# Kernel tuning notes

Measured on AMD Instinct MI355X. Metric: run time of the kernel, lower is better.

The kernel has to match this reference:

```python
import jax, jax.numpy as jnp
import numpy as np

B, N, C = 4, 4096, 512
H = 8          # num_heads
M = 64         # num_landmarks
HD = C // H    # head_dim = 64
N_ITER = 6     # Newton-Schulz iterations (Nystromformer default)


def iterative_inv(mat):
    # mat: [B, H, M, M]; Nystromformer pseudo-inverse via Newton-Schulz.
    I = jnp.eye(mat.shape[-1], dtype=mat.dtype)
    K = mat
    # global-max initialization (original Nystromformer 'original' init)
    V = K.swapaxes(-1, -2) / (jnp.max(jnp.sum(K, axis=-2)) * jnp.max(jnp.sum(K, axis=-1)))
    for _ in range(N_ITER):
        KV = jnp.matmul(K, V)
        V = 0.25 * jnp.matmul(V, 13.0 * I - jnp.matmul(KV, 15.0 * I - jnp.matmul(KV, 7.0 * I - KV)))
    return V


def setup_inputs() -> dict:
    key = jax.random.key(0)
    k1, k2, k3, k4 = jax.random.split(key, 4)
    s = C ** -0.5
    return {
        "x": jax.random.normal(k1, (B, N, C), dtype=jnp.float32),
        "qkv_w": jax.random.normal(k2, (3 * C, C), dtype=jnp.float32) * s,
        "proj_w": jax.random.normal(k3, (C, C), dtype=jnp.float32) * s,
        "proj_b": jax.random.normal(k4, (C,), dtype=jnp.float32) * 0.01,
        "epoch": 1,
    }


def reference(x, qkv_w, proj_w, proj_b, epoch):
    b, n, c = x.shape
    hd = c // H
    qkv = (x @ qkv_w.T).reshape(b, n, 3, H, hd).transpose(2, 0, 3, 1, 4)  # [3,B,H,N,hd]
    Q, K, V = qkv[0], qkv[1], qkv[2]
    scale = 1.0 / np.sqrt(np.sqrt(hd)).astype(np.float32)
    Q = Q * scale
    K = K * scale
    # landmark pooling: mean over segments of length N // M
    Ql = Q.reshape(b, H, M, n // M, hd).mean(axis=-2)  # [B,H,M,hd]
    Kl = K.reshape(b, H, M, n // M, hd).mean(axis=-2)
    kernel_1 = jax.nn.softmax(jnp.einsum('bhnd,bhmd->bhnm', Q, Kl), axis=-1)   # [B,H,N,M]
    kernel_2 = jax.nn.softmax(jnp.einsum('bhmd,bhld->bhml', Ql, Kl), axis=-1)  # [B,H,M,M]
    kernel_3 = jax.nn.softmax(jnp.einsum('bhmd,bhnd->bhmn', Ql, K), axis=-1)   # [B,H,M,N]
    X = jnp.matmul(jnp.matmul(kernel_1, iterative_inv(kernel_2)), jnp.matmul(kernel_3, V))
    X = X.transpose(0, 2, 1, 3).reshape(b, n, c)
    return X @ proj_w.T + proj_b
```

## Files before the change

kernel.cpp:

```cpp
#include <hip/hip_runtime.h>
#include <hip/hip_bf16.h>
#include <stdint.h>

#define QSZe 8388608ull

typedef __attribute__((ext_vector_type(8))) short bf16x8;
typedef __attribute__((ext_vector_type(4))) float f32x4;
typedef const __attribute__((address_space(1))) unsigned int* gas1_t;
typedef __attribute__((address_space(3))) unsigned int* las3_t;

__device__ __forceinline__ float bf2f(unsigned short u) {
  return __uint_as_float(((unsigned int)u) << 16);
}
__device__ __forceinline__ unsigned short f2bf(float f) {
  unsigned int u = __float_as_uint(f);
  unsigned int r = (u + 0x7FFFu + ((u >> 16) & 1u)) >> 16;
  return (unsigned short)r;
}
__device__ __forceinline__ void gload_lds16(const void* g, void* l) {
  __builtin_amdgcn_global_load_lds((gas1_t)g, (las3_t)l, 16, 0, 0);
}

__global__ void detect_dtype(const unsigned short* __restrict__ raw,
                             unsigned int* __restrict__ flag) {
  int t = threadIdx.x;
  int big = 0;
  for (int i = t; i < 256; i += 64) {
    int e = (raw[i] >> 7) & 0xFF;
    if (e >= 0x8F) big = 1;
  }
  unsigned long long b = __ballot(big);
  if (t == 0) flag[0] = (b != 0ull) ? 1u : 0u;
}

__global__ __launch_bounds__(256) void convert_bf16(
    const void* __restrict__ raw, unsigned short* __restrict__ canon, int n,
    const unsigned int* __restrict__ flag) {
  int i8 = (blockIdx.x * 256 + threadIdx.x) * 8;
  if (i8 >= n) return;
  if (flag[0]) {
    const float* f = (const float*)raw;
    float4 a = *(const float4*)(f + i8);
    float4 b = *(const float4*)(f + i8 + 4);
    unsigned short o[8] = {f2bf(a.x), f2bf(a.y), f2bf(a.z), f2bf(a.w),
                           f2bf(b.x), f2bf(b.y), f2bf(b.z), f2bf(b.w)};
    *(uint4*)(canon + i8) = *(const uint4*)o;
  } else {
    *(uint4*)(canon + i8) = *(const uint4*)((const unsigned short*)raw + i8);
  }
}

__global__ __launch_bounds__(256) void convert_f32(
    const void* __restrict__ raw, float* __restrict__ canon, int n,
    const unsigned int* __restrict__ flag) {
  int i = blockIdx.x * 256 + threadIdx.x;
  if (i >= n) return;
  canon[i] = flag[0] ? ((const float*)raw)[i]
                     : bf2f(((const unsigned short*)raw)[i]);
}

__device__ __forceinline__ void mmB(const unsigned short* A_R,
                                    const unsigned short* B_T,
                                    unsigned short* out_R,
                                    unsigned short* out_T, int wave, int lane,
                                    float s, float dg, float a7,
                                    const unsigned short* Aelt) {
  const int fr = lane & 15, fq = lane >> 4;
  bf16x8 af0 = *(const bf16x8*)&A_R[(wave * 16 + fr) * 64 + fq * 8];
  bf16x8 af1 = *(const bf16x8*)&A_R[(wave * 16 + fr) * 64 + 32 + fq * 8];
  f32x4 acc[4] = {};
#pragma unroll
  for (int j = 0; j < 4; j++) {
    bf16x8 b0 = *(const bf16x8*)&B_T[(j * 16 + fr) * 64 + fq * 8];
    bf16x8 b1 = *(const bf16x8*)&B_T[(j * 16 + fr) * 64 + 32 + fq * 8];
    acc[j] = __builtin_amdgcn_mfma_f32_16x16x32_bf16(af0, b0, acc[j], 0, 0, 0);
    acc[j] = __builtin_amdgcn_mfma_f32_16x16x32_bf16(af1, b1, acc[j], 0, 0, 0);
  }
  float ael[4][4];
  if (Aelt) {
#pragma unroll
    for (int j = 0; j < 4; j++)
#pragma unroll
      for (int r = 0; r < 4; r++)
        ael[j][r] = bf2f(Aelt[(wave * 16 + fq * 4 + r) * 64 + j * 16 + fr]);
  }
  __syncthreads();
#pragma unroll
  for (int j = 0; j < 4; j++) {
    int col = j * 16 + fr;
    unsigned short pack[4];
#pragma unroll
    for (int r = 0; r < 4; r++) {
      int row = wave * 16 + fq * 4 + r;
      float v = s * acc[j][r] + ((row == col) ? dg : 0.0f);
      if (Aelt) v += a7 * ael[j][r];
      unsigned short bv = f2bf(v);
      if (out_R) out_R[row * 64 + col] = bv;
      pack[r] = bv;
    }
    if (out_T)
      *(uint2*)&out_T[col * 64 + wave * 16 + fq * 4] = *(const uint2*)pack;
  }
}

__global__ __launch_bounds__(256) void qkv_gemm_mfma(
    const unsigned short* __restrict__ x, const unsigned short* __restrict__ w,
    unsigned short* __restrict__ qkv) {
  __shared__ __align__(16) unsigned short At[128 * 64];
  __shared__ __align__(16) unsigned short Bt[128 * 64];
  const int t = threadIdx.x;
  const int lane = t & 63, wave = t >> 6;
  const int wr = wave >> 1, wc = wave & 1;
  const int i0 = blockIdx.y * 128, j0 = blockIdx.x * 128;
  const int srow = lane >> 3;
  const int skc = (lane & 7) * 8;
  const int fr = lane & 15, fq = lane >> 4;
  f32x4 acc[4][4] = {};

  for (int k0 = 0; k0 < 512; k0 += 64) {
#pragma unroll
    for (int s = 0; s < 4; s++) {
      int inst = wave * 4 + s;
      int row = inst * 8 + srow;
      gload_lds16(x + (size_t)(i0 + row) * 512 + k0 + skc, &At[inst * 512]);
      gload_lds16(w + (size_t)(j0 + row) * 512 + k0 + skc, &Bt[inst * 512]);
    }
    __syncthreads();
#pragma unroll
    for (int kk = 0; kk < 64; kk += 32) {
      bf16x8 af[4], bg[4];
#pragma unroll
      for (int i = 0; i < 4; i++)
        af[i] = *(const bf16x8*)&At[(wr * 64 + i * 16 + fr) * 64 + kk + fq * 8];
#pragma unroll
      for (int j = 0; j < 4; j++)
        bg[j] = *(const bf16x8*)&Bt[(wc * 64 + j * 16 + fr) * 64 + kk + fq * 8];
#pragma unroll
      for (int i = 0; i < 4; i++)
#pragma unroll
        for (int j = 0; j < 4; j++)
          acc[i][j] = __builtin_amdgcn_mfma_f32_16x16x32_bf16(
              af[i], bg[j], acc[i][j], 0, 0, 0);
    }
    __syncthreads();
  }
#pragma unroll
  for (int j = 0; j < 4; j++) {
    int col = j0 + wc * 64 + j * 16 + fr;
    int which = col >> 9;
    int h = (col >> 6) & 7;
    int d = col & 63;
    float scale = (which < 2) ? 0.3535533905932738f : 1.0f;
#pragma unroll
    for (int i = 0; i < 4; i++) {
      int rbase = i0 + wr * 64 + i * 16 + fq * 4;
#pragma unroll
      for (int r = 0; r < 4; r++) {
        int row = rbase + r;
        int b_ = row >> 12, n = row & 4095;
        qkv[(size_t)which * QSZe + ((size_t)(b_ * 8 + h) * 4096 + n) * 64 + d] =
            f2bf(acc[i][j][r] * scale);
      }
    }
  }
}

__global__ __launch_bounds__(256) void pool_kernel(
    const unsigned short* __restrict__ qkv, float* __restrict__ Ql,
    float* __restrict__ Kl, unsigned short* __restrict__ Klb,
    unsigned short* __restrict__ Qlb) {
  int idx = blockIdx.x * 256 + threadIdx.x;
  int d = idx & 63;
  int m = (idx >> 6) & 63;
  int bh = idx >> 12;
  const unsigned short* qb =
      qkv + (size_t)bh * 262144 + (size_t)m * 4096 + d;
  const unsigned short* kb = qb + QSZe;
  float sq = 0.f, sk = 0.f;
#pragma unroll 8
  for (int tok = 0; tok < 64; tok++) {
    sq += bf2f(qb[tok * 64]);
    sk += bf2f(kb[tok * 64]);
  }
  float qv = sq * (1.0f / 64.0f);
  float kv = sk * (1.0f / 64.0f);
  Ql[idx] = qv;
  Kl[idx] = kv;
  Klb[idx] = f2bf(kv);
  Qlb[idx] = f2bf(qv);
}

__global__ __launch_bounds__(256) void k2_kernel(
    const float* __restrict__ Ql, const float* __restrict__ Kl,
    float* __restrict__ k2, unsigned int* __restrict__ gstat) {
  __shared__ float KlT[64 * 64];
  __shared__ float Ps[64][65];
  int t = threadIdx.x;
  int lane = t & 63, wv = t >> 6;
  int bh = blockIdx.x;
#pragma unroll
  for (int i = 0; i < 16; i++) {
    int idx = i * 256 + t;
    KlT[(idx & 63) * 64 + (idx >> 6)] = Kl[bh * 4096 + idx];
  }
  __syncthreads();
  for (int r = wv * 16; r < wv * 16 + 16; r++) {
    float qv = Ql[(bh * 64 + r) * 64 + lane];
    float acc = 0.f;
#pragma unroll
    for (int k = 0; k < 64; k++) acc += __shfl(qv, k, 64) * KlT[k * 64 + lane];
    float mx = acc;
#pragma unroll
    for (int o = 32; o > 0; o >>= 1) mx = fmaxf(mx, __shfl_xor(mx, o, 64));
    float e = __expf(acc - mx);
    float s = e;
#pragma unroll
    for (int o = 32; o > 0; o >>= 1) s += __shfl_xor(s, o, 64);
    float p = e / s;
    k2[(bh * 64 + r) * 64 + lane] = p;
    Ps[r][lane] = p;
  }
  __syncthreads();
  float val = 0.f;
  if (t < 64) {
    for (int r = 0; r < 64; r++) val += Ps[r][t];
  } else if (t < 128) {
    int r = t - 64;
    for (int c = 0; c < 64; c++) val += Ps[r][c];
  }
  float mv = val;
#pragma unroll
  for (int o = 32; o > 0; o >>= 1) mv = fmaxf(mv, __shfl_xor(mv, o, 64));
  if (t == 0) atomicMax(gstat + 0, __float_as_uint(mv));
  if (t == 64) atomicMax(gstat + 1, __float_as_uint(mv));
}

__global__ __launch_bounds__(256) void k3_mfma(
    const unsigned short* __restrict__ Qlb,
    const unsigned short* __restrict__ qkv, float* __restrict__ Wp,
    float* __restrict__ sp) {
  __shared__ __align__(16) unsigned short Et[64 * 136];
  __shared__ __align__(16) unsigned short Vt[64 * 136];
  __shared__ float scol_l[4][64];
  const int t = threadIdx.x;
  const int lane = t & 63, wave = t >> 6;
  const int fr = lane & 15, fq = lane >> 4;
  const int slab = blockIdx.x, bh = blockIdx.y;
  const int n_base = slab * 512;
  const unsigned short* Kb = qkv + QSZe + (size_t)bh * 262144;
  const unsigned short* Vb = qkv + 2 * QSZe + (size_t)bh * 262144;
  const unsigned short* Qlp = Qlb + bh * 4096;

  bf16x8 qb[2][4];
#pragma unroll
  for (int h = 0; h < 2; h++)
#pragma unroll
    for (int j = 0; j < 4; j++)
      qb[h][j] = *(const bf16x8*)(Qlp + (j * 16 + fr) * 64 + h * 32 + fq * 8);

  f32x4 accW[4] = {};
  float scol[4] = {0.f, 0.f, 0.f, 0.f};

  for (int sc = 0; sc < 4; sc++) {
    const int n0 = n_base + sc * 128;
    {
      int n = t & 127, dg = t >> 7;
#pragma unroll
      for (int i = 0; i < 4; i++) {
        int d0 = (dg + 2 * i) * 8;
        uint4 v = *(const uint4*)(Vb + (size_t)(n0 + n) * 64 + d0);
        const unsigned short* s = (const unsigned short*)&v;
#pragma unroll
        for (int u = 0; u < 8; u++) Vt[(d0 + u) * 136 + n] = s[u];
      }
    }
    f32x4 acc[2][4] = {};
#pragma unroll
    for (int i = 0; i < 2; i++) {
      const unsigned short* Kr =
          Kb + (size_t)(n0 + wave * 32 + i * 16 + fr) * 64;
      bf16x8 a0 = *(const bf16x8*)(Kr + fq * 8);
      bf16x8 a1 = *(const bf16x8*)(Kr + 32 + fq * 8);
#pragma unroll
      for (int j = 0; j < 4; j++) {
        acc[i][j] =
            __builtin_amdgcn_mfma_f32_16x16x32_bf16(a0, qb[0][j], acc[i][j],
                                                    0, 0, 0);
        acc[i][j] =
            __builtin_amdgcn_mfma_f32_16x16x32_bf16(a1, qb[1][j], acc[i][j],
                                                    0, 0, 0);
      }
    }
#pragma unroll
    for (int i = 0; i < 2; i++)
#pragma unroll
      for (int j = 0; j < 4; j++) {
        unsigned short pack[4];
        float s4 = 0.f;
#pragma unroll
        for (int r = 0; r < 4; r++) {
          float e = __expf(acc[i][j][r]);
          s4 += e;
          pack[r] = f2bf(e);
        }
        scol[j] += s4;
        *(uint2*)&Et[(j * 16 + fr) * 136 + wave * 32 + i * 16 + fq * 4] =
            *(const uint2*)pack;
      }
    __syncthreads();
#pragma unroll
    for (int kk = 0; kk < 128; kk += 32) {
      bf16x8 ap = *(const bf16x8*)&Et[(wave * 16 + fr) * 136 + kk + fq * 8];
#pragma unroll
      for (int j = 0; j < 4; j++) {
        bf16x8 bv = *(const bf16x8*)&Vt[(j * 16 + fr) * 136 + kk + fq * 8];
        accW[j] =
            __builtin_amdgcn_mfma_f32_16x16x32_bf16(ap, bv, accW[j], 0, 0, 0);
      }
    }
    __syncthreads();
  }
#pragma unroll
  for (int j = 0; j < 4; j++) {
    float s = scol[j];
    s += __shfl_xor(s, 16, 64);
    s += __shfl_xor(s, 32, 64);
    if (fq == 0) scol_l[wave][j * 16 + fr] = s;
  }
  __syncthreads();
  if (t < 64)
    sp[(bh * 8 + slab) * 64 + t] =
        scol_l[0][t] + scol_l[1][t] + scol_l[2][t] + scol_l[3][t];
  float* wpo = Wp + ((size_t)bh * 8 + slab) * 4096;
#pragma unroll
  for (int j = 0; j < 4; j++)
#pragma unroll
    for (int r = 0; r < 4; r++)
      wpo[(wave * 16 + fq * 4 + r) * 64 + j * 16 + fr] = accW[j][r];
}

__global__ __launch_bounds__(256) void k3_reduce(
    const float* __restrict__ Wp, const float* __restrict__ sp,
    float* __restrict__ W) {
  int idx = blockIdx.x * 256 + threadIdx.x;
  int m = (idx >> 6) & 63, bh = idx >> 12;
  float w = 0.f, s = 0.f;
#pragma unroll
  for (int c = 0; c < 8; c++) {
    w += Wp[((size_t)bh * 8 + c) * 4096 + (idx & 4095)];
    s += sp[(bh * 8 + c) * 64 + m];
  }
  W[idx] = w / s;
}

__global__ __launch_bounds__(256) void ns_kernel(
    const float* __restrict__ k2g, const unsigned int* __restrict__ gstat,
    const float* __restrict__ Wg, unsigned short* __restrict__ Ztb) {
  __shared__ __align__(16) unsigned short L[8 * 4096];
  unsigned short* K2R = L;
  unsigned short* VR = L + 4096;
  unsigned short* VT = L + 2 * 4096;
  unsigned short* AR = L + 3 * 4096;
  unsigned short* AT = L + 4 * 4096;
  unsigned short* T2T = L + 5 * 4096;
  unsigned short* T3T = L + 6 * 4096;
  unsigned short* WT = L + 7 * 4096;
  const int t = threadIdx.x, bh = blockIdx.x;
  const int lane = t & 63, wave = t >> 6;
  const float scale =
      1.0f / (__uint_as_float(gstat[0]) * __uint_as_float(gstat[1]));
  const float* k2p = k2g + bh * 4096;
  const float* wp = Wg + bh * 4096;
#pragma unroll
  for (int i = 0; i < 16; i++) {
    int idx = i * 256 + t;
    int r = idx >> 6, c = idx & 63;
    float kv = k2p[idx];
    K2R[idx] = f2bf(kv);
    VT[idx] = f2bf(kv * scale);
    VR[idx] = f2bf(k2p[c * 64 + r] * scale);
    WT[idx] = f2bf(wp[c * 64 + r]);
  }
  __syncthreads();
  for (int it = 0; it < 6; it++) {
    mmB(K2R, VT, AR, AT, wave, lane, 1.0f, 0.0f, 0.0f, nullptr);
    __syncthreads();
    mmB(AR, AT, nullptr, T2T, wave, lane, 1.0f, 15.0f, -7.0f, AR);
    __syncthreads();
    mmB(AR, T2T, nullptr, T3T, wave, lane, -1.0f, 13.0f, 0.0f, nullptr);
    __syncthreads();
    mmB(VR, T3T, VR, VT, wave, lane, 0.25f, 0.0f, 0.0f, nullptr);
    __syncthreads();
  }
  {
    const int fr = lane & 15, fq = lane >> 4;
    bf16x8 af0 = *(const bf16x8*)&WT[(wave * 16 + fr) * 64 + fq * 8];
    bf16x8 af1 = *(const bf16x8*)&WT[(wave * 16 + fr) * 64 + 32 + fq * 8];
    f32x4 acc[4] = {};
#pragma unroll
    for (int j = 0; j < 4; j++) {
      bf16x8 b0 = *(const bf16x8*)&VR[(j * 16 + fr) * 64 + fq * 8];
      bf16x8 b1 = *(const bf16x8*)&VR[(j * 16 + fr) * 64 + 32 + fq * 8];
      acc[j] =
          __builtin_amdgcn_mfma_f32_16x16x32_bf16(af0, b0, acc[j], 0, 0, 0);
      acc[j] =
          __builtin_amdgcn_mfma_f32_16x16x32_bf16(af1, b1, acc[j], 0, 0, 0);
    }
#pragma unroll
    for (int j = 0; j < 4; j++) {
      int m = j * 16 + fr;
#pragma unroll
      for (int r = 0; r < 4; r++) {
        int d = wave * 16 + fq * 4 + r;
        Ztb[bh * 4096 + d * 64 + m] = f2bf(acc[j][r]);
      }
    }
  }
}

__global__ __launch_bounds__(256) void k1x_mfma(
    const unsigned short* __restrict__ qkv,
    const unsigned short* __restrict__ Klb,
    const unsigned short* __restrict__ Ztb, unsigned short* __restrict__ X) {
  __shared__ __align__(16) unsigned short Qt[128 * 64];
  __shared__ __align__(16) unsigned short Ps[128 * 72];
  const int t = threadIdx.x;
  const int lane = t & 63, wave = t >> 6;
  const int fr = lane & 15, fq = lane >> 4;
  const int bh = blockIdx.x;
  const int n0 = blockIdx.y * 128;
  const unsigned short* Qb = qkv + (size_t)bh * 262144 + (size_t)n0 * 64;
  const unsigned short* Klp = Klb + bh * 4096;
  const unsigned short* Ztp = Ztb + bh * 4096;

  {
    const int srow = lane >> 3, skc = (lane & 7) * 8;
#pragma unroll
    for (int s = 0; s < 4; s++) {
      int inst = wave * 4 + s;
      gload_lds16(Qb + (size_t)(inst * 8 + srow) * 64 + skc, &Qt[inst * 512]);
    }
  }
  __syncthreads();

  f32x4 acc[2][4] = {};
#pragma unroll
  for (int kk = 0; kk < 64; kk += 32) {
    bf16x8 af[2], bg[4];
#pragma unroll
    for (int i = 0; i < 2; i++)
      af[i] =
          *(const bf16x8*)&Qt[(wave * 32 + i * 16 + fr) * 64 + kk + fq * 8];
#pragma unroll
    for (int j = 0; j < 4; j++)
      bg[j] = *(const bf16x8*)(Klp + (j * 16 + fr) * 64 + kk + fq * 8);
#pragma unroll
    for (int i = 0; i < 2; i++)
#pragma unroll
      for (int j = 0; j < 4; j++)
        acc[i][j] = __builtin_amdgcn_mfma_f32_16x16x32_bf16(af[i], bg[j],
                                                            acc[i][j], 0, 0, 0);
  }

#pragma unroll
  for (int i = 0; i < 2; i++) {
    float sr[4] = {0.f, 0.f, 0.f, 0.f};
#pragma unroll
    for (int j = 0; j < 4; j++)
#pragma unroll
      for (int r = 0; r < 4; r++) {
        float e = __expf(acc[i][j][r]);
        acc[i][j][r] = e;
        sr[r] += e;
      }
#pragma unroll
    for (int mask = 1; mask < 16; mask <<= 1)
#pragma unroll
      for (int r = 0; r < 4; r++) sr[r] += __shfl_xor(sr[r], mask, 64);
    float is[4];
#pragma unroll
    for (int r = 0; r < 4; r++) is[r] = 1.0f / sr[r];
#pragma unroll
    for (int j = 0; j < 4; j++)
#pragma unroll
      for (int r = 0; r < 4; r++)
        Ps[(wave * 32 + i * 16 + fq * 4 + r) * 72 + j * 16 + fr] =
            f2bf(acc[i][j][r] * is[r]);
  }
  __syncthreads();

  f32x4 ax[2][4] = {};
#pragma unroll
  for (int kk = 0; kk < 64; kk += 32) {
    bf16x8 ap[2], bz[4];
#pragma unroll
    for (int i = 0; i < 2; i++)
      ap[i] =
          *(const bf16x8*)&Ps[(wave * 32 + i * 16 + fr) * 72 + kk + fq * 8];
#pragma unroll
    for (int j = 0; j < 4; j++)
      bz[j] = *(const bf16x8*)(Ztp + (j * 16 + fr) * 64 + kk + fq * 8);
#pragma unroll
    for (int i = 0; i < 2; i++)
#pragma unroll
      for (int j = 0; j < 4; j++)
        ax[i][j] = __builtin_amdgcn_mfma_f32_16x16x32_bf16(ap[i], bz[j],
                                                           ax[i][j], 0, 0, 0);
  }

  const int b_ = bh >> 3, h = bh & 7;
#pragma unroll
  for (int i = 0; i < 2; i++) {
#pragma unroll
    for (int j = 0; j < 4; j++) {
      int c = h * 64 + j * 16 + fr;
#pragma unroll
      for (int r = 0; r < 4; r++) {
        int n = n0 + wave * 32 + i * 16 + fq * 4 + r;
        X[((size_t)(b_ * 4096 + n)) * 512 + c] = f2bf(ax[i][j][r]);
      }
    }
  }
}

__global__ __launch_bounds__(256) void proj_gemm_mfma(
    const unsigned short* __restrict__ X, const unsigned short* __restrict__ w,
    const float* __restrict__ bias, float* __restrict__ out) {
  __shared__ __align__(16) unsigned short At[128 * 64];
  __shared__ __align__(16) unsigned short Bt[128 * 64];
  const int t = threadIdx.x;
  const int lane = t & 63, wave = t >> 6;
  const int wr = wave >> 1, wc = wave & 1;
  const int i0 = blockIdx.y * 128, j0 = blockIdx.x * 128;
  const int srow = lane >> 3;
  const int skc = (lane & 7) * 8;
  const int fr = lane & 15, fq = lane >> 4;
  f32x4 acc[4][4] = {};

  for (int k0 = 0; k0 < 512; k0 += 64) {
#pragma unroll
    for (int s = 0; s < 4; s++) {
      int inst = wave * 4 + s;
      int row = inst * 8 + srow;
      gload_lds16(X + (size_t)(i0 + row) * 512 + k0 + skc, &At[inst * 512]);
      gload_lds16(w + (size_t)(j0 + row) * 512 + k0 + skc, &Bt[inst * 512]);
    }
    __syncthreads();
#pragma unroll
    for (int kk = 0; kk < 64; kk += 32) {
      bf16x8 af[4], bg[4];
#pragma unroll
      for (int i = 0; i < 4; i++)
        af[i] = *(const bf16x8*)&At[(wr * 64 + i * 16 + fr) * 64 + kk + fq * 8];
#pragma unroll
      for (int j = 0; j < 4; j++)
        bg[j] = *(const bf16x8*)&Bt[(wc * 64 + j * 16 + fr) * 64 + kk + fq * 8];
#pragma unroll
      for (int i = 0; i < 4; i++)
#pragma unroll
        for (int j = 0; j < 4; j++)
          acc[i][j] = __builtin_amdgcn_mfma_f32_16x16x32_bf16(
              af[i], bg[j], acc[i][j], 0, 0, 0);
    }
    __syncthreads();
  }
#pragma unroll
  for (int j = 0; j < 4; j++) {
    int col = j0 + wc * 64 + j * 16 + fr;
    float bia = bias[col];
#pragma unroll
    for (int i = 0; i < 4; i++) {
      int rbase = i0 + wr * 64 + i * 16 + fq * 4;
#pragma unroll
      for (int r = 0; r < 4; r++) {
        out[(size_t)(rbase + r) * 512 + col] = acc[i][j][r] + bia;
      }
    }
  }
}

extern "C" void kernel_launch(void* const* d_in, const int* in_sizes, int n_in,
                              void* d_out, int out_size, void* d_ws,
                              size_t ws_size, hipStream_t stream) {
  (void)in_sizes; (void)n_in; (void)out_size; (void)ws_size;

  char* w8 = (char*)d_ws;
  unsigned short* cx  = (unsigned short*)(w8 + 0);
  unsigned short* cwq = (unsigned short*)(w8 + 16777216);
  unsigned short* cwp = (unsigned short*)(w8 + 18350080);
  float*          cbf = (float*)(w8 + 18874368);
  unsigned short* qkv = (unsigned short*)(w8 + 18876416);
  unsigned short* X   = (unsigned short*)(w8 + 69208064);
  float* Ql = (float*)(w8 + 85985280);
  float* Kl = (float*)(w8 + 86509568);
  float* k2 = (float*)(w8 + 87033856);
  float* W  = (float*)(w8 + 87558144);
  unsigned short* Ztb = (unsigned short*)(w8 + 88082432);
  unsigned int* gstat = (unsigned int*)(w8 + 88606720);
  float* Wp = (float*)(w8 + 88608768);
  float* sp = (float*)(w8 + 92803072);
  unsigned short* Klb = (unsigned short*)(w8 + 92868608);
  unsigned short* Qlb = (unsigned short*)(w8 + 93130752);

  hipMemsetAsync(gstat, 0, 16, stream);
  detect_dtype<<<1, 64, 0, stream>>>((const unsigned short*)d_in[0],
                                     gstat + 2);
  convert_bf16<<<4096, 256, 0, stream>>>(d_in[0], cx, 8388608, gstat + 2);
  convert_bf16<<<384, 256, 0, stream>>>(d_in[1], cwq, 786432, gstat + 2);
  convert_bf16<<<128, 256, 0, stream>>>(d_in[2], cwp, 262144, gstat + 2);
  convert_f32<<<2, 256, 0, stream>>>(d_in[3], cbf, 512, gstat + 2);

  qkv_gemm_mfma<<<dim3(12, 128), 256, 0, stream>>>(cx, cwq, qkv);
  pool_kernel<<<512, 256, 0, stream>>>(qkv, Ql, Kl, Klb, Qlb);
  k2_kernel<<<32, 256, 0, stream>>>(Ql, Kl, k2, gstat);
  k3_mfma<<<dim3(8, 32), 256, 0, stream>>>(Qlb, qkv, Wp, sp);
  k3_reduce<<<512, 256, 0, stream>>>(Wp, sp, W);
  ns_kernel<<<32, 256, 0, stream>>>(k2, gstat, W, Ztb);
  k1x_mfma<<<dim3(32, 32), 256, 0, stream>>>(qkv, Klb, Ztb, X);
  proj_gemm_mfma<<<dim3(4, 128), 256, 0, stream>>>(X, cwp, cbf,
                                                   (float*)d_out);
}
```

Baseline: 255.3 us.

## Fuse landmark pooling into QKV GEMM epilogue and merge conversion/reduce kernels

The QKV GEMM is transposed so each wave's accumulator tile covers a whole 64-token segment of one head. The epilogue can then compute the landmark means by a cross-lane shuffle reduction and write Ql/Kl directly, which removes the separate pool kernel's re-read of Q and K. The epilogue also writes qkv as packed 4-element stores along the head dimension. In addition, the three bf16 conversions become one kernel, bias conversion moves into the dtype-detect kernel, and the k3_reduce kernel is folded into the ns_kernel prologue, cutting launches and an intermediate buffer. The risk is extra shuffle and register work in the GEMM epilogue, plus the ns_kernel prologue now doing eight strided global reads per element.

```diff
diff --git a/kernel.cpp b/kernel.cpp
--- a/kernel.cpp
+++ b/kernel.cpp
@@ -21,42 +21,57 @@
   __builtin_amdgcn_global_load_lds((gas1_t)g, (las3_t)l, 16, 0, 0);
 }
 
-__global__ void detect_dtype(const unsigned short* __restrict__ raw,
-                             unsigned int* __restrict__ flag) {
+__global__ void detect_bias(const unsigned short* __restrict__ raw_x,
+                            const void* __restrict__ raw_b,
+                            float* __restrict__ cbf,
+                            unsigned int* __restrict__ flag) {
+  __shared__ unsigned int fl;
   int t = threadIdx.x;
-  int big = 0;
-  for (int i = t; i < 256; i += 64) {
-    int e = (raw[i] >> 7) & 0xFF;
-    if (e >= 0x8F) big = 1;
-  }
-  unsigned long long b = __ballot(big);
-  if (t == 0) flag[0] = (b != 0ull) ? 1u : 0u;
-}
-
-__global__ __launch_bounds__(256) void convert_bf16(
-    const void* __restrict__ raw, unsigned short* __restrict__ canon, int n,
+  if (t < 64) {
+    int big = 0;
+    for (int i = t; i < 256; i += 64) {
+      int e = (raw_x[i] >> 7) & 0xFF;
+      if (e >= 0x8F) big = 1;
+    }
+    unsigned long long b = __ballot(big);
+    if (t == 0) {
+      fl = (b != 0ull) ? 1u : 0u;
+      flag[0] = fl;
+    }
+  }
+  __syncthreads();
+  unsigned int f = fl;
+  for (int i = t; i < 512; i += 256)
+    cbf[i] = f ? ((const float*)raw_b)[i]
+               : bf2f(((const unsigned short*)raw_b)[i]);
+}
+
+__global__ __launch_bounds__(256) void conv_all(
+    const void* __restrict__ rx, const void* __restrict__ rwq,
+    const void* __restrict__ rwp, unsigned short* __restrict__ cx,
+    unsigned short* __restrict__ cwq, unsigned short* __restrict__ cwp,
     const unsigned int* __restrict__ flag) {
-  int i8 = (blockIdx.x * 256 + threadIdx.x) * 8;
-  if (i8 >= n) return;
+  int gid = blockIdx.x * 256 + threadIdx.x;
+  const void* src;
+  unsigned short* dst;
+  int i8;
+  if (gid < 1048576) {
+    src = rx; dst = cx; i8 = gid * 8;
+  } else if (gid < 1146880) {
+    src = rwq; dst = cwq; i8 = (gid - 1048576) * 8;
+  } else {
+    src = rwp; dst = cwp; i8 = (gid - 1146880) * 8;
+  }
   if (flag[0]) {
-    const float* f = (const float*)raw;
+    const float* f = (const float*)src;
     float4 a = *(const float4*)(f + i8);
     float4 b = *(const float4*)(f + i8 + 4);
     unsigned short o[8] = {f2bf(a.x), f2bf(a.y), f2bf(a.z), f2bf(a.w),
                            f2bf(b.x), f2bf(b.y), f2bf(b.z), f2bf(b.w)};
-    *(uint4*)(canon + i8) = *(const uint4*)o;
+    *(uint4*)(dst + i8) = *(const uint4*)o;
   } else {
-    *(uint4*)(canon + i8) = *(const uint4*)((const unsigned short*)raw + i8);
-  }
-}
-
-__global__ __launch_bounds__(256) void convert_f32(
-    const void* __restrict__ raw, float* __restrict__ canon, int n,
-    const unsigned int* __restrict__ flag) {
-  int i = blockIdx.x * 256 + threadIdx.x;
-  if (i >= n) return;
-  canon[i] = flag[0] ? ((const float*)raw)[i]
-                     : bf2f(((const unsigned short*)raw)[i]);
+    *(uint4*)(dst + i8) = *(const uint4*)((const unsigned short*)src + i8);
+  }
 }
 
 __device__ __forceinline__ void mmB(const unsigned short* A_R,
@@ -104,16 +119,17 @@
 }
 
 __global__ __launch_bounds__(256) void qkv_gemm_mfma(
-    const unsigned short* __restrict__ x, const unsigned short* __restrict__ w,
-    unsigned short* __restrict__ qkv) {
+    const unsigned short* __restrict__ w, const unsigned short* __restrict__ x,
+    unsigned short* __restrict__ qkv, float* __restrict__ Ql,
+    float* __restrict__ Kl, unsigned short* __restrict__ Qlb,
+    unsigned short* __restrict__ Klb) {
   __shared__ __align__(16) unsigned short At[128 * 64];
   __shared__ __align__(16) unsigned short Bt[128 * 64];
   const int t = threadIdx.x;
   const int lane = t & 63, wave = t >> 6;
-  const int wr = wave >> 1, wc = wave & 1;
-  const int i0 = blockIdx.y * 128, j0 = blockIdx.x * 128;
-  const int srow = lane >> 3;
-  const int skc = (lane & 7) * 8;
+  const int wf = wave >> 1, wt = wave & 1;
+  const int f0 = blockIdx.x * 128, n0g = blockIdx.y * 128;
+  const int srow = lane >> 3, skc = (lane & 7) * 8;
   const int fr = lane & 15, fq = lane >> 4;
   f32x4 acc[4][4] = {};
 
@@ -122,72 +138,76 @@
     for (int s = 0; s < 4; s++) {
       int inst = wave * 4 + s;
       int row = inst * 8 + srow;
-      gload_lds16(x + (size_t)(i0 + row) * 512 + k0 + skc, &At[inst * 512]);
-      gload_lds16(w + (size_t)(j0 + row) * 512 + k0 + skc, &Bt[inst * 512]);
+      gload_lds16(w + (size_t)(f0 + row) * 512 + k0 + skc, &At[inst * 512]);
+      gload_lds16(x + (size_t)(n0g + row) * 512 + k0 + skc, &Bt[inst * 512]);
     }
     __syncthreads();
 #pragma unroll
     for (int kk = 0; kk < 64; kk += 32) {
-      bf16x8 af[4], bg[4];
+      bf16x8 af[4], bxf[4];
 #pragma unroll
       for (int i = 0; i < 4; i++)
-        af[i] = *(const bf16x8*)&At[(wr * 64 + i * 16 + fr) * 64 + kk + fq * 8];
+        af[i] = *(const bf16x8*)&At[(wf * 64 + i * 16 + fr) * 64 + kk + fq * 8];
 #pragma unroll
       for (int j = 0; j < 4; j++)
-        bg[j] = *(const bf16x8*)&Bt[(wc * 64 + j * 16 + fr) * 64 + kk + fq * 8];
+        bxf[j] =
+            *(const bf16x8*)&Bt[(wt * 64 + j * 16 + fr) * 64 + kk + fq * 8];
 #pragma unroll
       for (int i = 0; i < 4; i++)
 #pragma unroll
         for (int j = 0; j < 4; j++)
           acc[i][j] = __builtin_amdgcn_mfma_f32_16x16x32_bf16(
-              af[i], bg[j], acc[i][j], 0, 0, 0);
-    }
-    __syncthreads();
-  }
-#pragma unroll
-  for (int j = 0; j < 4; j++) {
-    int col = j0 + wc * 64 + j * 16 + fr;
-    int which = col >> 9;
-    int h = (col >> 6) & 7;
-    int d = col & 63;
-    float scale = (which < 2) ? 0.3535533905932738f : 1.0f;
+              af[i], bxf[j], acc[i][j], 0, 0, 0);
+    }
+    __syncthreads();
+  }
+  const int fbase = f0 + wf * 64;
+  const int which = fbase >> 9;
+  const int h = (fbase >> 6) & 7;
+  const float scale = (which < 2) ? 0.3535533905932738f : 1.0f;
+  const int b_ = n0g >> 12;
+  const int bh = b_ * 8 + h;
+  const int m_loc = ((n0g + wt * 64) & 4095) >> 6;
+#pragma unroll
+  for (int i = 0; i < 4; i++) {
+    int d0 = i * 16 + fq * 4;
+#pragma unroll
+    for (int j = 0; j < 4; j++) {
+      int nn = (n0g + wt * 64 + j * 16 + fr) & 4095;
+      unsigned short pack[4];
+#pragma unroll
+      for (int r = 0; r < 4; r++) pack[r] = f2bf(acc[i][j][r] * scale);
+      *(uint2*)&qkv[(size_t)which * QSZe + ((size_t)bh * 4096 + nn) * 64 +
+                    d0] = *(const uint2*)pack;
+    }
+  }
+  if (which < 2) {
+    const float ps = scale * (1.0f / 64.0f);
 #pragma unroll
     for (int i = 0; i < 4; i++) {
-      int rbase = i0 + wr * 64 + i * 16 + fq * 4;
-#pragma unroll
-      for (int r = 0; r < 4; r++) {
-        int row = rbase + r;
-        int b_ = row >> 12, n = row & 4095;
-        qkv[(size_t)which * QSZe + ((size_t)(b_ * 8 + h) * 4096 + n) * 64 + d] =
-            f2bf(acc[i][j][r] * scale);
-      }
-    }
-  }
-}
-
-__global__ __launch_bounds__(256) void pool_kernel(
-    const unsigned short* __restrict__ qkv, float* __restrict__ Ql,
-    float* __restrict__ Kl, unsigned short* __restrict__ Klb,
-    unsigned short* __restrict__ Qlb) {
-  int idx = blockIdx.x * 256 + threadIdx.x;
-  int d = idx & 63;
-  int m = (idx >> 6) & 63;
-  int bh = idx >> 12;
-  const unsigned short* qb =
-      qkv + (size_t)bh * 262144 + (size_t)m * 4096 + d;
-  const unsigned short* kb = qb + QSZe;
-  float sq = 0.f, sk = 0.f;
-#pragma unroll 8
-  for (int tok = 0; tok < 64; tok++) {
-    sq += bf2f(qb[tok * 64]);
-    sk += bf2f(kb[tok * 64]);
-  }
-  float qv = sq * (1.0f / 64.0f);
-  float kv = sk * (1.0f / 64.0f);
-  Ql[idx] = qv;
-  Kl[idx] = kv;
-  Klb[idx] = f2bf(kv);
-  Qlb[idx] = f2bf(qv);
+      float sm[4];
+#pragma unroll
+      for (int r = 0; r < 4; r++)
+        sm[r] = acc[i][0][r] + acc[i][1][r] + acc[i][2][r] + acc[i][3][r];
+#pragma unroll
+      for (int mask = 1; mask < 16; mask <<= 1)
+#pragma unroll
+        for (int r = 0; r < 4; r++) sm[r] += __shfl_xor(sm[r], mask, 64);
+      if (fr == 0) {
+        int d0 = i * 16 + fq * 4;
+        float4 v4 = make_float4(sm[0] * ps, sm[1] * ps, sm[2] * ps, sm[3] * ps);
+        unsigned short pk[4] = {f2bf(v4.x), f2bf(v4.y), f2bf(v4.z), f2bf(v4.w)};
+        size_t off = (size_t)bh * 4096 + m_loc * 64 + d0;
+        if (which == 0) {
+          *(float4*)&Ql[off] = v4;
+          *(uint2*)&Qlb[off] = *(const uint2*)pk;
+        } else {
+          *(float4*)&Kl[off] = v4;
+          *(uint2*)&Klb[off] = *(const uint2*)pk;
+        }
+      }
+    }
+  }
 }
 
 __global__ __launch_bounds__(256) void k2_kernel(
@@ -283,12 +303,10 @@
       bf16x8 a1 = *(const bf16x8*)(Kr + 32 + fq * 8);
 #pragma unroll
       for (int j = 0; j < 4; j++) {
-        acc[i][j] =
-            __builtin_amdgcn_mfma_f32_16x16x32_bf16(a0, qb[0][j], acc[i][j],
-                                                    0, 0, 0);
-        acc[i][j] =
-            __builtin_amdgcn_mfma_f32_16x16x32_bf16(a1, qb[1][j], acc[i][j],
-                                                    0, 0, 0);
+        acc[i][j] = __builtin_amdgcn_mfma_f32_16x16x32_bf16(a0, qb[0][j],
+                                                            acc[i][j], 0, 0, 0);
+        acc[i][j] = __builtin_amdgcn_mfma_f32_16x16x32_bf16(a1, qb[1][j],
+                                                            acc[i][j], 0, 0, 0);
       }
     }
 #pragma unroll
@@ -339,24 +357,12 @@
       wpo[(wave * 16 + fq * 4 + r) * 64 + j * 16 + fr] = accW[j][r];
 }
 
-__global__ __launch_bounds__(256) void k3_reduce(
-    const float* __restrict__ Wp, const float* __restrict__ sp,
-    float* __restrict__ W) {
-  int idx = blockIdx.x * 256 + threadIdx.x;
-  int m = (idx >> 6) & 63, bh = idx >> 12;
-  float w = 0.f, s = 0.f;
-#pragma unroll
-  for (int c = 0; c < 8; c++) {
-    w += Wp[((size_t)bh * 8 + c) * 4096 + (idx & 4095)];
-    s += sp[(bh * 8 + c) * 64 + m];
-  }
-  W[idx] = w / s;
-}
-
 __global__ __launch_bounds__(256) void ns_kernel(
     const float* __restrict__ k2g, const unsigned int* __restrict__ gstat,
-    const float* __restrict__ Wg, unsigned short* __restrict__ Ztb) {
+    const float* __restrict__ Wp, const float* __restrict__ sp,
+    unsigned short* __restrict__ Ztb) {
   __shared__ __align__(16) unsigned short L[8 * 4096];
+  __shared__ float ssum[64];
   unsigned short* K2R = L;
   unsigned short* VR = L + 4096;
   unsigned short* VT = L + 2 * 4096;
@@ -370,16 +376,26 @@
   const float scale =
       1.0f / (__uint_as_float(gstat[0]) * __uint_as_float(gstat[1]));
   const float* k2p = k2g + bh * 4096;
-  const float* wp = Wg + bh * 4096;
+  if (t < 64) {
+    float s = 0.f;
+#pragma unroll
+    for (int c = 0; c < 8; c++) s += sp[(bh * 8 + c) * 64 + t];
+    ssum[t] = s;
+  }
+  __syncthreads();
 #pragma unroll
   for (int i = 0; i < 16; i++) {
     int idx = i * 256 + t;
-    int r = idx >> 6, c = idx & 63;
+    int m = idx >> 6, d = idx & 63;
     float kv = k2p[idx];
     K2R[idx] = f2bf(kv);
     VT[idx] = f2bf(kv * scale);
-    VR[idx] = f2bf(k2p[c * 64 + r] * scale);
-    WT[idx] = f2bf(wp[c * 64 + r]);
+    VR[idx] = f2bf(k2p[d * 64 + m] * scale);
+    float wv = 0.f;
+#pragma unroll
+    for (int cc = 0; cc < 8; cc++)
+      wv += Wp[((size_t)(bh * 8 + cc)) * 4096 + idx];
+    WT[d * 64 + m] = f2bf(wv / ssum[m]);
   }
   __syncthreads();
   for (int it = 0; it < 6; it++) {
@@ -594,7 +610,6 @@
   float* Ql = (float*)(w8 + 85985280);
   float* Kl = (float*)(w8 + 86509568);
   float* k2 = (float*)(w8 + 87033856);
-  float* W  = (float*)(w8 + 87558144);
   unsigned short* Ztb = (unsigned short*)(w8 + 88082432);
   unsigned int* gstat = (unsigned int*)(w8 + 88606720);
   float* Wp = (float*)(w8 + 88608768);
@@ -603,19 +618,15 @@
   unsigned short* Qlb = (unsigned short*)(w8 + 93130752);
 
   hipMemsetAsync(gstat, 0, 16, stream);
-  detect_dtype<<<1, 64, 0, stream>>>((const unsigned short*)d_in[0],
+  detect_bias<<<1, 256, 0, stream>>>((const unsigned short*)d_in[0], d_in[3],
+                                     cbf, gstat + 2);
+  conv_all<<<4608, 256, 0, stream>>>(d_in[0], d_in[1], d_in[2], cx, cwq, cwp,
                                      gstat + 2);
-  convert_bf16<<<4096, 256, 0, stream>>>(d_in[0], cx, 8388608, gstat + 2);
-  convert_bf16<<<384, 256, 0, stream>>>(d_in[1], cwq, 786432, gstat + 2);
-  convert_bf16<<<128, 256, 0, stream>>>(d_in[2], cwp, 262144, gstat + 2);
-  convert_f32<<<2, 256, 0, stream>>>(d_in[3], cbf, 512, gstat + 2);
-
-  qkv_gemm_mfma<<<dim3(12, 128), 256, 0, stream>>>(cx, cwq, qkv);
-  pool_kernel<<<512, 256, 0, stream>>>(qkv, Ql, Kl, Klb, Qlb);
+  qkv_gemm_mfma<<<dim3(12, 128), 256, 0, stream>>>(cwq, cx, qkv, Ql, Kl, Qlb,
+                                                   Klb);
   k2_kernel<<<32, 256, 0, stream>>>(Ql, Kl, k2, gstat);
   k3_mfma<<<dim3(8, 32), 256, 0, stream>>>(Qlb, qkv, Wp, sp);
-  k3_reduce<<<512, 256, 0, stream>>>(Wp, sp, W);
-  ns_kernel<<<32, 256, 0, stream>>>(k2, gstat, W, Ztb);
+  ns_kernel<<<32, 256, 0, stream>>>(k2, gstat, Wp, sp, Ztb);
   k1x_mfma<<<dim3(32, 32), 256, 0, stream>>>(qkv, Klb, Ztb, X);
   proj_gemm_mfma<<<dim3(4, 128), 256, 0, stream>>>(X, cwp, cbf,
                                                    (float*)d_out);
```

Measured after the change: 249.5 us. 2.3% less time.
